# Kernel tuning notes

Hardware: AMD Instinct MI355X
Metric: run time of the kernel (lower is better)

The kernel has to match this reference:

```python
import jax, jax.numpy as jnp
import numpy as np

HIDDEN = 2048
REDUCTION = 4
DOWN = HIDDEN // REDUCTION  # 512
E = 16
K = 2
B, S = 4, 2048


def setup_inputs() -> dict:
    key = jax.random.key(0)
    k1, k2, k3, k4 = jax.random.split(key, 4)
    x = jax.random.normal(k1, (B, S, HIDDEN), dtype=jnp.float32)
    gate_w = jax.random.normal(k2, (E, HIDDEN), dtype=jnp.float32) * 0.02
    # xavier_uniform over (E, DOWN, HIDDEN): bound = sqrt(6/(DOWN+HIDDEN))
    bound = float(np.sqrt(6.0 / (DOWN + HIDDEN)))
    down_w = jax.random.uniform(k3, (E, DOWN, HIDDEN), dtype=jnp.float32,
                                minval=-bound, maxval=bound)
    down_b = jnp.zeros((E, DOWN), dtype=jnp.float32)
    ub = float(np.sqrt(1.0 / DOWN))
    up_w = jax.random.uniform(k4, (HIDDEN, DOWN), dtype=jnp.float32,
                              minval=-ub, maxval=ub)
    up_b = jnp.zeros((HIDDEN,), dtype=jnp.float32)
    return {"x": x, "gate_w": gate_w, "down_w": down_w, "down_b": down_b,
            "up_w": up_w, "up_b": up_b}


def reference(x, gate_w, down_w, down_b, up_w, up_b):
    Bb, Ss, D = x.shape
    N = Bb * Ss
    xf = x.reshape(N, D)
    # TopKGate: logits -> top-k -> softmax over the k logits -> scatter to full [N,E]
    logits = xf @ gate_w.T                       # [N, E]
    topv, topi = jax.lax.top_k(logits, K)        # [N, K]
    probs = jax.nn.softmax(topv, axis=-1)        # [N, K]
    gw = jnp.zeros_like(logits).at[jnp.arange(N)[:, None], topi].set(probs)  # [N, E]
    # Dense-equivalent of gather + per-token bmm + scatter-add combine:
    # final[n] = sum_e gw[n,e] * (down_w[e] @ x[n] + down_b[e])
    expert_out = jnp.einsum('nd,eod->neo', xf, down_w) + down_b[None]  # [N, E, DOWN]
    combined = jnp.einsum('ne,neo->no', gw, expert_out)                # [N, DOWN]
    h = jax.nn.gelu(combined, approximate=True)  # gelu_new (tanh approx)
    h = h.reshape(Bb, Ss, DOWN)
    out = h @ up_w.T + up_b                      # [B, S, HIDDEN]
    # load balancing loss: E * sum(sum(gw,0)/N * mean(gw,0)) * alpha
    loss = E * jnp.sum(jnp.sum(gw, axis=0) / N * jnp.mean(gw, axis=0)) * 0.1
    return out, loss
```

## Files before the change

### kernel.cpp

```cpp
#include <hip/hip_runtime.h>
#include <hip/hip_bf16.h>
#include <math.h>

#define NTOK   8192
#define HID    2048
#define DWN    512
#define NEXP   16
#define PADSLOT 18432
#define NSLOTBLK 144
#define DGRID_HALF (NSLOTBLK * (DWN / 256))

#define OFF_XB       0
#define OFF_DWB      33554432
#define OFF_H        33554432
#define OFF_UWB      67108864
#define OFF_TOK      69206016
#define OFF_SPOS     69279744
#define OFF_EIDX     69345280
#define OFF_PVAL     69410816
#define OFF_COUNTS   69476352
#define OFF_BASE     69476416
#define OFF_CURSOR   69476544
#define OFF_COLSUM   69476608
#define OFF_SEG      69476672
#define SEGHALF_SHORTS 9437184
#define SEGHALF_BYTES  18874368
#define WS_NEED1     (OFF_SEG + 1 * SEGHALF_BYTES)
#define WS_NEED2     (OFF_SEG + 2 * SEGHALF_BYTES)

typedef __attribute__((ext_vector_type(8))) __bf16 bf16x8;
typedef __attribute__((ext_vector_type(4))) float f32x4;

#define ASYNC16(gsrc, ldst) \
  __builtin_amdgcn_global_load_lds((const __attribute__((address_space(1))) unsigned int*)(gsrc), \
                                   (__attribute__((address_space(3))) unsigned int*)(ldst), 16, 0, 0)

__device__ inline unsigned short f2bf(float f) {
  unsigned int u = __float_as_uint(f);
  unsigned int r = (u + 0x7FFFu + ((u >> 16) & 1u)) >> 16;
  return (unsigned short)r;
}
__device__ inline float bf2f(unsigned short s) {
  return __uint_as_float((unsigned int)s << 16);
}

__global__ __launch_bounds__(256) void cast8_kernel(const float* __restrict__ src,
                                                    unsigned short* __restrict__ dst)
{
  size_t i = ((size_t)blockIdx.x * 256 + threadIdx.x) * 8;
  float4 a = *(const float4*)(src + i);
  float4 b = *(const float4*)(src + i + 4);
  unsigned short o[8];
  o[0]=f2bf(a.x); o[1]=f2bf(a.y); o[2]=f2bf(a.z); o[3]=f2bf(a.w);
  o[4]=f2bf(b.x); o[5]=f2bf(b.y); o[6]=f2bf(b.z); o[7]=f2bf(b.w);
  *(uint4*)(dst + i) = *(const uint4*)o;
}

__global__ __launch_bounds__(256, 4) void gate_kernel(
    const float* __restrict__ x, const float* __restrict__ gw,
    int2* __restrict__ eidx, float2* __restrict__ pvals,
    unsigned short* __restrict__ xbw)
{
  __shared__ float gws[2][NEXP * 256];

  int lane = threadIdx.x & 63;
  int wave = threadIdx.x >> 6;
  int n0 = (blockIdx.x * 4 + wave) * 2;
  const float* xr0 = x + (size_t)n0 * HID;
  const float* xr1 = xr0 + HID;
  unsigned short* xw0 = xbw + (size_t)n0 * HID;
  unsigned short* xw1 = xw0 + HID;

  double acc0[NEXP], acc1[NEXP];
#pragma unroll
  for (int e = 0; e < NEXP; e++) { acc0[e] = 0.0; acc1[e] = 0.0; }

#pragma unroll
  for (int r = 0; r < 4; r++) {
    int e = r * 4 + wave;
    ASYNC16(gw + (size_t)e * HID + lane * 4, &gws[0][e * 256]);
  }
  __syncthreads();

  int cur = 0;
  for (int c = 0; c < HID / 256; c++) {
    int d0 = c * 256;
    if (c + 1 < HID / 256) {
#pragma unroll
      for (int r = 0; r < 4; r++) {
        int e = r * 4 + wave;
        ASYNC16(gw + (size_t)e * HID + d0 + 256 + lane * 4, &gws[cur ^ 1][e * 256]);
      }
    }
    int d = d0 + lane * 4;
    float4 xv0 = *(const float4*)(xr0 + d);
    float4 xv1 = *(const float4*)(xr1 + d);
    unsigned short o0[4] = {f2bf(xv0.x), f2bf(xv0.y), f2bf(xv0.z), f2bf(xv0.w)};
    unsigned short o1[4] = {f2bf(xv1.x), f2bf(xv1.y), f2bf(xv1.z), f2bf(xv1.w)};
    *(uint2*)(xw0 + d) = *(const uint2*)o0;
    *(uint2*)(xw1 + d) = *(const uint2*)o1;
    double x00 = (double)xv0.x, x01 = (double)xv0.y, x02 = (double)xv0.z, x03 = (double)xv0.w;
    double x10 = (double)xv1.x, x11 = (double)xv1.y, x12 = (double)xv1.z, x13 = (double)xv1.w;
    const float* gs = &gws[cur][lane * 4];
#pragma unroll
    for (int e = 0; e < NEXP; e++) {
      float4 g = *(const float4*)(gs + e * 256);
      double g0 = (double)g.x, g1 = (double)g.y, g2 = (double)g.z, g3 = (double)g.w;
      double s0 = acc0[e], s1 = acc1[e];
      s0 = fma(x00, g0, s0); s0 = fma(x01, g1, s0);
      s0 = fma(x02, g2, s0); s0 = fma(x03, g3, s0);
      s1 = fma(x10, g0, s1); s1 = fma(x11, g1, s1);
      s1 = fma(x12, g2, s1); s1 = fma(x13, g3, s1);
      acc0[e] = s0; acc1[e] = s1;
    }
    __syncthreads();
    cur ^= 1;
  }

#define RED(v) { v += __shfl_xor(v,32,64); v += __shfl_xor(v,16,64); v += __shfl_xor(v,8,64); \
                 v += __shfl_xor(v,4,64);  v += __shfl_xor(v,2,64);  v += __shfl_xor(v,1,64); }
#pragma unroll
  for (int e = 0; e < NEXP; e++) { RED(acc0[e]) RED(acc1[e]) }
#undef RED

#define TOPSEL(ACC, N) { \
    double v0 = -1e300, v1 = -1e300; int i0 = 0, i1 = 0; \
    _Pragma("unroll") \
    for (int e = 0; e < NEXP; e++) { \
      double v = ACC[e]; \
      if (v > v0) { v1 = v0; i1 = i0; v0 = v; i0 = e; } \
      else if (v > v1) { v1 = v; i1 = e; } \
    } \
    double ex = exp(v1 - v0); \
    double denom = 1.0 + ex; \
    eidx[N]  = make_int2(i0, i1); \
    pvals[N] = make_float2((float)(1.0 / denom), (float)(ex / denom)); \
  }
  if (lane == 0) TOPSEL(acc0, n0)
  if (lane == 1) TOPSEL(acc1, n0 + 1)
#undef TOPSEL
}

__global__ __launch_bounds__(256) void hist_kernel(
    const int2* __restrict__ eidx, const float2* __restrict__ pvals,
    int* __restrict__ counts, float* __restrict__ colsum)
{
  __shared__ int   cbin[NEXP];
  __shared__ float lbin[NEXP];
  if (threadIdx.x < NEXP) { cbin[threadIdx.x] = 0; lbin[threadIdx.x] = 0.f; }
  __syncthreads();
  int n = blockIdx.x * 256 + threadIdx.x;
  int2 e = eidx[n];
  float2 p = pvals[n];
  atomicAdd(&cbin[e.x], 1);  atomicAdd(&lbin[e.x], p.x);
  atomicAdd(&cbin[e.y], 1);  atomicAdd(&lbin[e.y], p.y);
  __syncthreads();
  if (threadIdx.x < NEXP) {
    atomicAdd(&counts[threadIdx.x], cbin[threadIdx.x]);
    atomicAdd(&colsum[threadIdx.x], lbin[threadIdx.x]);
  }
}

__global__ void scan_loss_kernel(const int* __restrict__ counts, int* __restrict__ base,
                                 const float* __restrict__ colsum, float* __restrict__ loss_out)
{
  if (threadIdx.x == 0 && blockIdx.x == 0) {
    int acc = 0;
    for (int e = 0; e < NEXP; e++) { base[e] = acc; acc += (counts[e] + 127) & ~127; }
    base[NEXP] = acc;
    double s = 0.0;
    for (int e = 0; e < NEXP; e++) { double c = (double)colsum[e]; s += c * c; }
    loss_out[0] = (float)(1.6 * s / ((double)NTOK * (double)NTOK));
  }
}

__global__ __launch_bounds__(256) void scatter_kernel(
    const int2* __restrict__ eidx, const int* __restrict__ base, int* __restrict__ cursor,
    int* __restrict__ tok, int2* __restrict__ spos)
{
  int n = blockIdx.x * 256 + threadIdx.x;
  int lane = threadIdx.x & 63;
  int2 e = eidx[n];
  int myE[2] = {e.x, e.y};
  int myPos[2];
#pragma unroll
  for (int s = 0; s < 2; s++) {
    int eq = myE[s];
#pragma unroll
    for (int q = 0; q < NEXP; q++) {
      unsigned long long m = __ballot(eq == q);
      if (eq == q) {
        int cnt = __popcll(m);
        int pre = __popcll(m & ((1ull << lane) - 1ull));
        int b = 0;
        if (pre == 0) b = atomicAdd(&cursor[q], cnt);
        int leader = __ffsll((long long)m) - 1;
        b = __shfl(b, leader, 64);
        int pos = base[q] + b + pre;
        tok[pos] = n;
        myPos[s] = pos;
      }
    }
  }
  spos[n] = make_int2(myPos[0], myPos[1]);
}

__global__ __launch_bounds__(512, 2) void down_mfma_kernel(
    const unsigned short* __restrict__ xb, const unsigned short* __restrict__ dwb,
    const int* __restrict__ base, const int* __restrict__ tok,
    unsigned short* __restrict__ seg, int kcount)
{
  __shared__ unsigned short smem[49152];

  int wg  = blockIdx.x;
  int cpx = gridDim.x >> 3;
  int logical = (wg & 7) * cpx + (wg >> 3);
  int kh      = logical / DGRID_HALF;
  int r       = logical % DGRID_HALF;
  int slot0   = (r >> 1) * 128;
  int out0    = (r & 1) * 256;

  if (slot0 >= base[NEXP]) return;
  int e = 0;
#pragma unroll
  for (int q = 1; q < NEXP; q++) if (base[q] <= slot0) e = q;
  int kbase = kh * kcount * 64;

  int tid = threadIdx.x;
  const int l = tid & 63, w = tid >> 6;
  const int wm = w & 1, wn = w >> 1;
  const int lm = l & 15, quad = l >> 4;

  const unsigned short* agp[2];
  const unsigned short* bgp[4];
#pragma unroll
  for (int i = 0; i < 2; i++) {
    int g = w * 2 + i;
    int rr = g * 8 + (l & 7);
    int kc = l >> 3;
    int t = tok[slot0 + rr];
    agp[i] = xb + (size_t)(t < 0 ? 0 : t) * HID + kbase + kc * 8;
  }
#pragma unroll
  for (int i = 0; i < 4; i++) {
    int g = w * 4 + i;
    int rr = g * 8 + (l & 7);
    int kc = l >> 3;
    bgp[i] = dwb + ((size_t)e * DWN + out0 + rr) * HID + kbase + kc * 8;
  }

  int am_off[4], bn_off[4];
#pragma unroll
  for (int mi = 0; mi < 4; mi++) {
    int m = wm * 64 + mi * 16 + lm;
    am_off[mi] = (m >> 3) * 512 + (m & 7) * 8 + quad * 64;
    int nn = wn * 64 + mi * 16 + lm;
    bn_off[mi] = (nn >> 3) * 512 + (nn & 7) * 8 + quad * 64;
  }

  f32x4 acc[4][4] = {};

#pragma unroll
  for (int i = 0; i < 2; i++) ASYNC16(agp[i], &smem[(w * 2 + i) * 512]);
#pragma unroll
  for (int i = 0; i < 4; i++) ASYNC16(bgp[i], &smem[8192 + (w * 4 + i) * 512]);
  __syncthreads();

  int cur = 0;
  for (int it = 0; it < kcount; it++) {
    unsigned short* As = smem + cur * 24576;
    unsigned short* Bs = As + 8192;
    if (it + 1 < kcount) {
      int k0 = (it + 1) * 64;
      unsigned short* Ap = smem + (cur ^ 1) * 24576;
#pragma unroll
      for (int i = 0; i < 2; i++) ASYNC16(agp[i] + k0, &Ap[(w * 2 + i) * 512]);
#pragma unroll
      for (int i = 0; i < 4; i++) ASYNC16(bgp[i] + k0, &Ap[8192 + (w * 4 + i) * 512]);
    }
#pragma unroll
    for (int kk = 0; kk < 2; kk++) {
      bf16x8 af[4], bfr[4];
#pragma unroll
      for (int mi = 0; mi < 4; mi++) af[mi]  = *(const bf16x8*)&As[am_off[mi] + kk * 256];
#pragma unroll
      for (int ni = 0; ni < 4; ni++) bfr[ni] = *(const bf16x8*)&Bs[bn_off[ni] + kk * 256];
#pragma unroll
      for (int mi = 0; mi < 4; mi++)
#pragma unroll
        for (int ni = 0; ni < 4; ni++)
          acc[mi][ni] = __builtin_amdgcn_mfma_f32_16x16x32_bf16(af[mi], bfr[ni], acc[mi][ni], 0, 0, 0);
    }
    __syncthreads();
    cur ^= 1;
  }

#pragma unroll
  for (int mi = 0; mi < 4; mi++)
#pragma unroll
    for (int reg = 0; reg < 4; reg++) {
      int m = wm * 64 + mi * 16 + quad * 4 + reg;
#pragma unroll
      for (int ni = 0; ni < 4; ni++) {
        int c = wn * 64 + ni * 16 + lm;
        smem[m * 264 + c] = f2bf(acc[mi][ni][reg]);
      }
    }
  __syncthreads();
#pragma unroll
  for (int it2 = 0; it2 < 8; it2++) {
    int chunk = it2 * 512 + tid;
    int row = chunk >> 5, off = (chunk & 31) * 8;
    uint4 v = *(const uint4*)&smem[row * 264 + off];
    *(uint4*)&seg[(size_t)kh * SEGHALF_SHORTS + (size_t)(slot0 + row) * 512 + out0 + off] = v;
  }
}

__global__ __launch_bounds__(256) void combine_gelu_kernel(
    const unsigned short* __restrict__ seg, const int2* __restrict__ spos,
    const float2* __restrict__ pv, const int2* __restrict__ eix,
    const float* __restrict__ db, unsigned short* __restrict__ h, int ksplit)
{
  int n = blockIdx.x * 4 + (threadIdx.x >> 6);
  int lane = threadIdx.x & 63;
  int c0 = lane * 8;
  int2 sp = spos[n];
  float2 p = pv[n];
  int2 e = eix[n];

  float d0[8] = {0,0,0,0,0,0,0,0}, d1[8] = {0,0,0,0,0,0,0,0};
  for (int hh = 0; hh < ksplit; hh++) {
    uint4 u0 = *(const uint4*)(seg + (size_t)hh * SEGHALF_SHORTS + (size_t)sp.x * 512 + c0);
    uint4 u1 = *(const uint4*)(seg + (size_t)hh * SEGHALF_SHORTS + (size_t)sp.y * 512 + c0);
    const unsigned short* s0 = (const unsigned short*)&u0;
    const unsigned short* s1 = (const unsigned short*)&u1;
#pragma unroll
    for (int j = 0; j < 8; j++) { d0[j] += bf2f(s0[j]); d1[j] += bf2f(s1[j]); }
  }
  float b0[8], b1[8];
  *(float4*)&b0[0] = *(const float4*)(db + e.x * DWN + c0);
  *(float4*)&b0[4] = *(const float4*)(db + e.x * DWN + c0 + 4);
  *(float4*)&b1[0] = *(const float4*)(db + e.y * DWN + c0);
  *(float4*)&b1[4] = *(const float4*)(db + e.y * DWN + c0 + 4);

  unsigned short o[8];
#pragma unroll
  for (int j = 0; j < 8; j++) {
    float xx = p.x * (d0[j] + b0[j]) + p.y * (d1[j] + b1[j]);
    float inner = 0.7978845608028654f * (xx + 0.044715f * xx * xx * xx);
    o[j] = f2bf(0.5f * xx * (1.0f + tanhf(inner)));
  }
  *(uint4*)(h + (size_t)n * DWN + c0) = *(const uint4*)o;
}

__global__ __launch_bounds__(512, 2) void up_mfma_kernel(
    const unsigned short* __restrict__ h, const unsigned short* __restrict__ uwb,
    const float* __restrict__ ub, float* __restrict__ out)
{
  __shared__ unsigned short smem[65536];

  int wg  = blockIdx.x;
  int cpx = gridDim.x >> 3;
  int logical = (wg & 7) * cpx + (wg >> 3);
  int row0 = (logical >> 3) * 256;
  int col0 = (logical & 7) * 256;

  int tid = threadIdx.x;
  const int l = tid & 63, w = tid >> 6;
  const int wm = w & 1, wn = w >> 1;
  const int lm = l & 15, quad = l >> 4;

  const unsigned short* agp[4];
  const unsigned short* bgp[4];
#pragma unroll
  for (int i = 0; i < 4; i++) {
    int g = w * 4 + i;
    int rr = g * 8 + (l & 7);
    int kc = l >> 3;
    agp[i] = h   + (size_t)(row0 + rr) * DWN + kc * 8;
    bgp[i] = uwb + (size_t)(col0 + rr) * DWN + kc * 8;
  }

  int am_off[8], bn_off[4];
#pragma unroll
  for (int mi = 0; mi < 8; mi++) {
    int m = wm * 128 + mi * 16 + lm;
    am_off[mi] = (m >> 3) * 512 + (m & 7) * 8 + quad * 64;
  }
#pragma unroll
  for (int ni = 0; ni < 4; ni++) {
    int nn = wn * 64 + ni * 16 + lm;
    bn_off[ni] = (nn >> 3) * 512 + (nn & 7) * 8 + quad * 64;
  }

  f32x4 acc[8][4] = {};

#pragma unroll
  for (int i = 0; i < 4; i++) {
    int g = w * 4 + i;
    ASYNC16(agp[i], &smem[g * 512]);
    ASYNC16(bgp[i], &smem[16384 + g * 512]);
  }
  __syncthreads();

  int cur = 0;
  for (int k0 = 0; k0 < DWN; k0 += 64) {
    unsigned short* As = smem + cur * 32768;
    unsigned short* Bs = As + 16384;
    if (k0 + 64 < DWN) {
      unsigned short* Ap = smem + (cur ^ 1) * 32768;
#pragma unroll
      for (int i = 0; i < 4; i++) {
        int g = w * 4 + i;
        ASYNC16(agp[i] + k0 + 64, &Ap[g * 512]);
        ASYNC16(bgp[i] + k0 + 64, &Ap[16384 + g * 512]);
      }
    }
#pragma unroll
    for (int kk = 0; kk < 2; kk++) {
      bf16x8 af[8], bfr[4];
#pragma unroll
      for (int mi = 0; mi < 8; mi++) af[mi]  = *(const bf16x8*)&As[am_off[mi] + kk * 256];
#pragma unroll
      for (int ni = 0; ni < 4; ni++) bfr[ni] = *(const bf16x8*)&Bs[bn_off[ni] + kk * 256];
#pragma unroll
      for (int mi = 0; mi < 8; mi++)
#pragma unroll
        for (int ni = 0; ni < 4; ni++)
          acc[mi][ni] = __builtin_amdgcn_mfma_f32_16x16x32_bf16(af[mi], bfr[ni], acc[mi][ni], 0, 0, 0);
    }
    __syncthreads();
    cur ^= 1;
  }

  float ubv[4];
#pragma unroll
  for (int ni = 0; ni < 4; ni++)
    ubv[ni] = ub[col0 + wn * 64 + ni * 16 + lm];
#pragma unroll
  for (int mi = 0; mi < 8; mi++) {
#pragma unroll
    for (int reg = 0; reg < 4; reg++) {
      int m = row0 + wm * 128 + mi * 16 + quad * 4 + reg;
      float* orow = out + (size_t)m * HID;
#pragma unroll
      for (int ni = 0; ni < 4; ni++) {
        int gc = col0 + wn * 64 + ni * 16 + lm;
        orow[gc] = acc[mi][ni][reg] + ubv[ni];
      }
    }
  }
}

extern "C" void kernel_launch(void* const* d_in, const int* in_sizes, int n_in,
                              void* d_out, int out_size, void* d_ws, size_t ws_size,
                              hipStream_t stream)
{
  const float* x  = (const float*)d_in[0];
  const float* gw = (const float*)d_in[1];
  const float* dw = (const float*)d_in[2];
  const float* db = (const float*)d_in[3];
  const float* uw = (const float*)d_in[4];
  const float* ub = (const float*)d_in[5];
  float* out = (float*)d_out;

  char* ws = (char*)d_ws;
  unsigned short* xb   = (unsigned short*)(ws + OFF_XB);
  unsigned short* dwb  = (unsigned short*)(ws + OFF_DWB);
  unsigned short* uwb  = (unsigned short*)(ws + OFF_UWB);
  unsigned short* h    = (unsigned short*)(ws + OFF_H);
  unsigned short* seg  = (unsigned short*)(ws + OFF_SEG);
  int*    tok    = (int*)(ws + OFF_TOK);
  int2*   spos   = (int2*)(ws + OFF_SPOS);
  int2*   eidx   = (int2*)(ws + OFF_EIDX);
  float2* pvals  = (float2*)(ws + OFF_PVAL);
  int*    counts = (int*)(ws + OFF_COUNTS);
  int*    base   = (int*)(ws + OFF_BASE);
  int*    cursor = (int*)(ws + OFF_CURSOR);
  float*  colsum = (float*)(ws + OFF_COLSUM);

  const int ksplit = (ws_size >= (size_t)WS_NEED2) ? 2 : 1;
  const int kcount = (HID / 64) / ksplit;

  hipMemsetAsync(tok, 0xFF, PADSLOT * sizeof(int), stream);
  hipMemsetAsync(counts, 0, 320, stream);

  cast8_kernel<<<(NEXP * DWN * HID) / 8 / 256, 256, 0, stream>>>(dw, dwb);
  cast8_kernel<<<(HID * DWN) / 8 / 256, 256, 0, stream>>>(uw, uwb);

  gate_kernel<<<NTOK / 8, 256, 0, stream>>>(x, gw, eidx, pvals, xb);
  hist_kernel<<<NTOK / 256, 256, 0, stream>>>(eidx, pvals, counts, colsum);
  scan_loss_kernel<<<1, 64, 0, stream>>>(counts, base, colsum, out + (size_t)NTOK * HID);
  scatter_kernel<<<NTOK / 256, 256, 0, stream>>>(eidx, base, cursor, tok, spos);

  down_mfma_kernel<<<DGRID_HALF * ksplit, 512, 0, stream>>>(xb, dwb, base, tok, seg, kcount);

  combine_gelu_kernel<<<NTOK / 4, 256, 0, stream>>>(seg, spos, pvals, eidx, db, h, ksplit);

  up_mfma_kernel<<<(NTOK / 256) * (HID / 256), 512, 0, stream>>>(h, uwb, ub, out);
}
```

Before: 394.9 us.

## Restructure GEMM main loops with two-stage prefetch, vmcnt waits and setprio

Result: faster. 374.2 us (-5.2%).

```diff
diff --git a/kernel.cpp b/kernel.cpp
--- a/kernel.cpp
+++ b/kernel.cpp
@@ -35,6 +35,10 @@
   __builtin_amdgcn_global_load_lds((const __attribute__((address_space(1))) unsigned int*)(gsrc), \
                                    (__attribute__((address_space(3))) unsigned int*)(ldst), 16, 0, 0)
 
+#define VMWAIT_BAR(N) do { asm volatile("s_waitcnt vmcnt(" #N ")" ::: "memory"); \
+                           __builtin_amdgcn_s_barrier(); } while (0)
+#define NOSTMT ((void)0)
+
 __device__ inline unsigned short f2bf(float f) {
   unsigned int u = __float_as_uint(f);
   unsigned int r = (u + 0x7FFFu + ((u >> 16) & 1u)) >> 16;
@@ -260,41 +264,61 @@
 
   f32x4 acc[4][4] = {};
 
-#pragma unroll
-  for (int i = 0; i < 2; i++) ASYNC16(agp[i], &smem[(w * 2 + i) * 512]);
-#pragma unroll
-  for (int i = 0; i < 4; i++) ASYNC16(bgp[i], &smem[8192 + (w * 4 + i) * 512]);
+#define DSTAGE(BUF, T) do {                                                   \
+    int k0_ = (T) * 64;                                                       \
+    unsigned short* Ap_ = smem + (BUF) * 24576;                               \
+    _Pragma("unroll") for (int i = 0; i < 2; i++)                             \
+      ASYNC16(agp[i] + k0_, &Ap_[(w * 2 + i) * 512]);                         \
+    _Pragma("unroll") for (int i = 0; i < 4; i++)                             \
+      ASYNC16(bgp[i] + k0_, &Ap_[8192 + (w * 4 + i) * 512]);                  \
+  } while (0)
+
+  DSTAGE(0, 0);
+  DSTAGE(1, 1);
+  asm volatile("s_waitcnt vmcnt(6)" ::: "memory");
+  __builtin_amdgcn_s_barrier();
+
+  int cur = 0;
+#define DTILE(STAGE_STMT, WAIT_STMT) do {                                     \
+    unsigned short* As = smem + cur * 24576;                                  \
+    unsigned short* Bs = As + 8192;                                           \
+    bf16x8 a0[4], b0[4], a1[4], b1[4];                                        \
+    _Pragma("unroll") for (int mi = 0; mi < 4; mi++) {                        \
+      a0[mi] = *(const bf16x8*)&As[am_off[mi]];                               \
+      b0[mi] = *(const bf16x8*)&Bs[bn_off[mi]];                               \
+    }                                                                         \
+    __builtin_amdgcn_s_setprio(1);                                            \
+    _Pragma("unroll") for (int mi = 0; mi < 4; mi++)                          \
+      _Pragma("unroll") for (int ni = 0; ni < 4; ni++)                        \
+        acc[mi][ni] = __builtin_amdgcn_mfma_f32_16x16x32_bf16(a0[mi], b0[ni], acc[mi][ni], 0, 0, 0); \
+    __builtin_amdgcn_s_setprio(0);                                            \
+    _Pragma("unroll") for (int mi = 0; mi < 4; mi++) {                        \
+      a1[mi] = *(const bf16x8*)&As[am_off[mi] + 256];                         \
+      b1[mi] = *(const bf16x8*)&Bs[bn_off[mi] + 256];                         \
+    }                                                                         \
+    asm volatile("s_waitcnt lgkmcnt(0)" ::: "memory");                        \
+    __builtin_amdgcn_sched_barrier(0);                                        \
+    __builtin_amdgcn_s_barrier();           \
+    STAGE_STMT;                                                               \
+    __builtin_amdgcn_s_setprio(1);                                            \
+    _Pragma("unroll") for (int mi = 0; mi < 4; mi++)                          \
+      _Pragma("unroll") for (int ni = 0; ni < 4; ni++)                        \
+        acc[mi][ni] = __builtin_amdgcn_mfma_f32_16x16x32_bf16(a1[mi], b1[ni], acc[mi][ni], 0, 0, 0); \
+    __builtin_amdgcn_s_setprio(0);                                            \
+    WAIT_STMT;                                                                \
+  } while (0)
+
+  for (int it = 0; it < kcount - 2; ++it) {
+    DTILE(DSTAGE(cur, it + 2), VMWAIT_BAR(6));
+    cur ^= 1;
+  }
+  DTILE(NOSTMT, VMWAIT_BAR(0));
+  cur ^= 1;
+  DTILE(NOSTMT, NOSTMT);
+#undef DTILE
+#undef DSTAGE
+
   __syncthreads();
-
-  int cur = 0;
-  for (int it = 0; it < kcount; it++) {
-    unsigned short* As = smem + cur * 24576;
-    unsigned short* Bs = As + 8192;
-    if (it + 1 < kcount) {
-      int k0 = (it + 1) * 64;
-      unsigned short* Ap = smem + (cur ^ 1) * 24576;
-#pragma unroll
-      for (int i = 0; i < 2; i++) ASYNC16(agp[i] + k0, &Ap[(w * 2 + i) * 512]);
-#pragma unroll
-      for (int i = 0; i < 4; i++) ASYNC16(bgp[i] + k0, &Ap[8192 + (w * 4 + i) * 512]);
-    }
-#pragma unroll
-    for (int kk = 0; kk < 2; kk++) {
-      bf16x8 af[4], bfr[4];
-#pragma unroll
-      for (int mi = 0; mi < 4; mi++) af[mi]  = *(const bf16x8*)&As[am_off[mi] + kk * 256];
-#pragma unroll
-      for (int ni = 0; ni < 4; ni++) bfr[ni] = *(const bf16x8*)&Bs[bn_off[ni] + kk * 256];
-#pragma unroll
-      for (int mi = 0; mi < 4; mi++)
-#pragma unroll
-        for (int ni = 0; ni < 4; ni++)
-          acc[mi][ni] = __builtin_amdgcn_mfma_f32_16x16x32_bf16(af[mi], bfr[ni], acc[mi][ni], 0, 0, 0);
-    }
-    __syncthreads();
-    cur ^= 1;
-  }
-
 #pragma unroll
   for (int mi = 0; mi < 4; mi++)
 #pragma unroll
@@ -395,43 +419,57 @@
 
   f32x4 acc[8][4] = {};
 
-#pragma unroll
-  for (int i = 0; i < 4; i++) {
-    int g = w * 4 + i;
-    ASYNC16(agp[i], &smem[g * 512]);
-    ASYNC16(bgp[i], &smem[16384 + g * 512]);
-  }
-  __syncthreads();
+#define USTAGE(BUF, T) do {                                                   \
+    int k0_ = (T) * 64;                                                       \
+    unsigned short* Ap_ = smem + (BUF) * 32768;                               \
+    _Pragma("unroll") for (int i = 0; i < 4; i++) {                           \
+      int g_ = w * 4 + i;                                                     \
+      ASYNC16(agp[i] + k0_, &Ap_[g_ * 512]);                                  \
+      ASYNC16(bgp[i] + k0_, &Ap_[16384 + g_ * 512]);                          \
+    }                                                                         \
+  } while (0)
+
+  USTAGE(0, 0);
+  USTAGE(1, 1);
+  asm volatile("s_waitcnt vmcnt(8)" ::: "memory");
+  __builtin_amdgcn_s_barrier();
 
   int cur = 0;
-  for (int k0 = 0; k0 < DWN; k0 += 64) {
-    unsigned short* As = smem + cur * 32768;
-    unsigned short* Bs = As + 16384;
-    if (k0 + 64 < DWN) {
-      unsigned short* Ap = smem + (cur ^ 1) * 32768;
-#pragma unroll
-      for (int i = 0; i < 4; i++) {
-        int g = w * 4 + i;
-        ASYNC16(agp[i] + k0 + 64, &Ap[g * 512]);
-        ASYNC16(bgp[i] + k0 + 64, &Ap[16384 + g * 512]);
-      }
-    }
-#pragma unroll
-    for (int kk = 0; kk < 2; kk++) {
-      bf16x8 af[8], bfr[4];
-#pragma unroll
-      for (int mi = 0; mi < 8; mi++) af[mi]  = *(const bf16x8*)&As[am_off[mi] + kk * 256];
-#pragma unroll
-      for (int ni = 0; ni < 4; ni++) bfr[ni] = *(const bf16x8*)&Bs[bn_off[ni] + kk * 256];
-#pragma unroll
-      for (int mi = 0; mi < 8; mi++)
-#pragma unroll
-        for (int ni = 0; ni < 4; ni++)
-          acc[mi][ni] = __builtin_amdgcn_mfma_f32_16x16x32_bf16(af[mi], bfr[ni], acc[mi][ni], 0, 0, 0);
-    }
-    __syncthreads();
+#define UTILE(STAGE_STMT, WAIT_STMT) do {                                     \
+    unsigned short* As = smem + cur * 32768;                                  \
+    unsigned short* Bs = As + 16384;                                          \
+    bf16x8 a0[8], b0[4], a1[8], b1[4];                                        \
+    _Pragma("unroll") for (int mi = 0; mi < 8; mi++) a0[mi] = *(const bf16x8*)&As[am_off[mi]]; \
+    _Pragma("unroll") for (int ni = 0; ni < 4; ni++) b0[ni] = *(const bf16x8*)&Bs[bn_off[ni]]; \
+    __builtin_amdgcn_s_setprio(1);                                            \
+    _Pragma("unroll") for (int mi = 0; mi < 8; mi++)                          \
+      _Pragma("unroll") for (int ni = 0; ni < 4; ni++)                        \
+        acc[mi][ni] = __builtin_amdgcn_mfma_f32_16x16x32_bf16(a0[mi], b0[ni], acc[mi][ni], 0, 0, 0); \
+    __builtin_amdgcn_s_setprio(0);                                            \
+    _Pragma("unroll") for (int mi = 0; mi < 8; mi++) a1[mi] = *(const bf16x8*)&As[am_off[mi] + 256]; \
+    _Pragma("unroll") for (int ni = 0; ni < 4; ni++) b1[ni] = *(const bf16x8*)&Bs[bn_off[ni] + 256]; \
+    asm volatile("s_waitcnt lgkmcnt(0)" ::: "memory");                        \
+    __builtin_amdgcn_sched_barrier(0);                                        \
+    __builtin_amdgcn_s_barrier();                                             \
+    STAGE_STMT;                                                               \
+    __builtin_amdgcn_s_setprio(1);                                            \
+    _Pragma("unroll") for (int mi = 0; mi < 8; mi++)                          \
+      _Pragma("unroll") for (int ni = 0; ni < 4; ni++)                        \
+        acc[mi][ni] = __builtin_amdgcn_mfma_f32_16x16x32_bf16(a1[mi], b1[ni], acc[mi][ni], 0, 0, 0); \
+    __builtin_amdgcn_s_setprio(0);                                            \
+    WAIT_STMT;                                                                \
+  } while (0)
+
+  const int nt = DWN / 64;
+  for (int it = 0; it < nt - 2; ++it) {
+    UTILE(USTAGE(cur, it + 2), VMWAIT_BAR(8));
     cur ^= 1;
   }
+  UTILE(NOSTMT, VMWAIT_BAR(0));
+  cur ^= 1;
+  UTILE(NOSTMT, NOSTMT);
+#undef UTILE
+#undef USTAGE
 
   float ubv[4];
 #pragma unroll
```
